# Kernel tuning notes

Hardware: AMD Instinct MI355X
Metric: run time of the kernel (lower is better)

Reference implementation:

```python
import jax, jax.numpy as jnp
import numpy as np

N_USER = 100000
N_SELLER = 50000
E = 640000
D_U = 128
D_S = 64
H = 128
B = 50000


def setup_inputs() -> dict:
    key = jax.random.key(0)
    ks = jax.random.split(key, 24)

    def w(k, shape):
        # Glorot-ish scaling by fan_in
        return jax.random.normal(k, shape, dtype=jnp.float32) / np.sqrt(shape[0])

    return {
        "x_user": jax.random.normal(ks[0], (N_USER, D_U), dtype=jnp.float32),
        "x_seller": jax.random.normal(ks[1], (N_SELLER, D_S), dtype=jnp.float32),
        "src_buy": jax.random.randint(ks[2], (E,), 0, N_USER),
        "dst_buy": jax.random.randint(ks[3], (E,), 0, N_SELLER),
        "src_rev": jax.random.randint(ks[4], (E,), 0, N_SELLER),
        "dst_rev": jax.random.randint(ks[5], (E,), 0, N_USER),
        "mask_user": jax.random.randint(ks[6], (B,), 0, N_USER),
        "mask_seller": jax.random.randint(ks[7], (B,), 0, N_SELLER),
        # layer 1: (user,buy,seller) conv: src=user(D_U), dst=seller(D_S)
        "Wl1_buy": w(ks[8], (D_U, H)), "Wr1_buy": w(ks[9], (D_S, H)),
        "b1_buy": jnp.zeros((H,), jnp.float32),
        # layer 1: (seller,bought by,user) conv: src=seller(D_S), dst=user(D_U)
        "Wl1_rev": w(ks[10], (D_S, H)), "Wr1_rev": w(ks[11], (D_U, H)),
        "b1_rev": jnp.zeros((H,), jnp.float32),
        # layer 2 (both node types now have H features)
        "Wl2_buy": w(ks[12], (H, H)), "Wr2_buy": w(ks[13], (H, H)),
        "b2_buy": jnp.zeros((H,), jnp.float32),
        "Wl2_rev": w(ks[14], (H, H)), "Wr2_rev": w(ks[15], (H, H)),
        "b2_rev": jnp.zeros((H,), jnp.float32),
        # final head: Linear(2H, 1)
        "Wlin": w(ks[16], (2 * H, 1)), "blin": jnp.zeros((1,), jnp.float32),
    }


def _sage(x_src, x_dst, src, dst, Wl, Wr, b):
    """PyG SAGEConv: lin_l(mean_j x_src[j]) + lin_r(x_dst); bias on aggr branch."""
    n_dst = x_dst.shape[0]
    agg = jax.ops.segment_sum(x_src[src], dst, num_segments=n_dst)      # [n_dst, d_src]
    cnt = jax.ops.segment_sum(jnp.ones(src.shape, x_src.dtype), dst, num_segments=n_dst)
    mean = agg / jnp.maximum(cnt, 1.0)[:, None]                          # mean aggr, 0 for isolated
    return mean @ Wl + b + x_dst @ Wr


def reference(x_user, x_seller, src_buy, dst_buy, src_rev, dst_rev,
              mask_user, mask_seller,
              Wl1_buy, Wr1_buy, b1_buy, Wl1_rev, Wr1_rev, b1_rev,
              Wl2_buy, Wr2_buy, b2_buy, Wl2_rev, Wr2_rev, b2_rev,
              Wlin, blin):
    # layer 1 (HeteroConv aggr='sum' is trivial: one relation per dst type)
    s1 = jax.nn.relu(_sage(x_user, x_seller, src_buy, dst_buy, Wl1_buy, Wr1_buy, b1_buy))
    u1 = jax.nn.relu(_sage(x_seller, x_user, src_rev, dst_rev, Wl1_rev, Wr1_rev, b1_rev))
    # layer 2
    s2 = jax.nn.relu(_sage(u1, s1, src_buy, dst_buy, Wl2_buy, Wr2_buy, b2_buy))
    u2 = jax.nn.relu(_sage(s1, u1, src_rev, dst_rev, Wl2_rev, Wr2_rev, b2_rev))
    # masked gather + concat + linear + sigmoid
    x = jnp.concatenate((u2[mask_user], s2[mask_seller]), axis=1)        # [B, 2H]
    return jax.nn.sigmoid(x @ Wlin + blin).reshape(-1)
```

## Files before the change

### kernel.cpp

```cpp
#include <hip/hip_runtime.h>

#define N_USER   100000
#define N_SELLER 50000
#define NEDGE    640000
#define DU       128
#define DS       64
#define HH       128
#define BSZ      50000

#define ECHUNK   2048
#define NBLK     313
#define PW       128
#define NPART_B  391
#define NPART_R  782

#define CVT_BLK  15625
#define PREP_BLK 448

#define NB1_BUY  391
#define NB1_REV  782
#define NB2      391

#define AGG1_BUY_BLK 12500
#define AGG1_REV_BLK 25000
#define AGG2_BLK     12500

typedef unsigned short ushort_t;
typedef __attribute__((ext_vector_type(4))) unsigned short u16x4;
typedef __attribute__((ext_vector_type(8))) unsigned short u16x8;
typedef __attribute__((ext_vector_type(8))) short bf16x8;
typedef __attribute__((ext_vector_type(4))) float f32x4;

__device__ __forceinline__ float bf2f(ushort_t u) {
  union { unsigned int i; float f; } v; v.i = ((unsigned int)u) << 16; return v.f;
}
__device__ __forceinline__ ushort_t f2bf(float f) {
  union { float f; unsigned int i; } v; v.f = f;
  unsigned int x = v.i;
  unsigned int r = x + 0x7FFFu + ((x >> 16) & 1u);
  return (ushort_t)(r >> 16);
}
__device__ __forceinline__ float u2f(unsigned int u) {
  union { unsigned int i; float f; } v; v.i = u; return v.f;
}

__global__ void __launch_bounds__(256) k_hist(
    const int* __restrict__ dst_buy, const int* __restrict__ dst_rev,
    int* __restrict__ H_buy, int* __restrict__ H_rev) {
  __shared__ int lh[NPART_R];
  int b = blockIdx.x, t = threadIdx.x;
  bool is_buy = b < NBLK;
  int bb = is_buy ? b : b - NBLK;
  const int* dst = is_buy ? dst_buy : dst_rev;
  int* H = is_buy ? H_buy : H_rev;
  int np = is_buy ? NPART_B : NPART_R;
  for (int i = t; i < np; i += 256) lh[i] = 0;
  __syncthreads();
  int base = bb * ECHUNK;
#pragma unroll
  for (int i = 0; i < 8; ++i) {
    int e = base + i * 256 + t;
    if (e < NEDGE) atomicAdd(&lh[dst[e] >> 7], 1);
  }
  __syncthreads();
  for (int p = t; p < np; p += 256) H[p * NBLK + bb] = lh[p];
}

__global__ void __launch_bounds__(256) k_rowscan(
    int* __restrict__ H_buy, int* __restrict__ H_rev,
    int* __restrict__ rowtot_buy, int* __restrict__ rowtot_rev) {
  __shared__ int lds[256];
  int p = blockIdx.x, t = threadIdx.x;
  int* H; int* rowtot; int row;
  if (p < NPART_B) { H = H_buy; rowtot = rowtot_buy; row = p; }
  else             { H = H_rev; rowtot = rowtot_rev; row = p - NPART_B; }
  int i0 = 2 * t, i1 = 2 * t + 1;
  int v0 = (i0 < NBLK) ? H[row * NBLK + i0] : 0;
  int v1 = (i1 < NBLK) ? H[row * NBLK + i1] : 0;
  int tot = v0 + v1;
  lds[t] = tot;
  __syncthreads();
  for (int d = 1; d < 256; d <<= 1) {
    int x = (t >= d) ? lds[t - d] : 0;
    __syncthreads();
    lds[t] += x;
    __syncthreads();
  }
  int excl = lds[t] - tot;
  if (i0 < NBLK) H[row * NBLK + i0] = excl;
  if (i1 < NBLK) H[row * NBLK + i1] = excl + v0;
  if (t == 255) rowtot[row] = lds[255];
}

__global__ void __launch_bounds__(256) k_colscan(
    const int* __restrict__ rowtot_buy, const int* __restrict__ rowtot_rev,
    int* __restrict__ pstart_buy, int* __restrict__ pstart_rev) {
  __shared__ int lds[256];
  const int* rt; int* ps; int n;
  if (blockIdx.x == 0) { rt = rowtot_buy; ps = pstart_buy; n = NPART_B; }
  else                 { rt = rowtot_rev; ps = pstart_rev; n = NPART_R; }
  int t = threadIdx.x;
  int v[4]; int tot = 0;
#pragma unroll
  for (int i = 0; i < 4; ++i) { int idx = t * 4 + i; v[i] = (idx < n) ? rt[idx] : 0; tot += v[i]; }
  lds[t] = tot;
  __syncthreads();
  for (int d = 1; d < 256; d <<= 1) {
    int x = (t >= d) ? lds[t - d] : 0;
    __syncthreads();
    lds[t] += x;
    __syncthreads();
  }
  int excl = lds[t] - tot;
#pragma unroll
  for (int i = 0; i < 4; ++i) {
    int idx = t * 4 + i;
    if (idx < n) { ps[idx] = excl; excl += v[i]; }
  }
  if (t == 255) ps[n] = lds[255];
}

__global__ void __launch_bounds__(256) k_scat_cvt_prep(
    const int* __restrict__ src_buy, const int* __restrict__ dst_buy,
    const int* __restrict__ src_rev, const int* __restrict__ dst_rev,
    const int* __restrict__ H_buy, const int* __restrict__ H_rev,
    const int* __restrict__ pstart_buy, const int* __restrict__ pstart_rev,
    unsigned int* __restrict__ part_buy, unsigned int* __restrict__ part_rev,
    const float* __restrict__ x_user, ushort_t* __restrict__ xu_bf,
    const float* __restrict__ x_seller, ushort_t* __restrict__ xs_bf,
    const float* __restrict__ Wl1b, const float* __restrict__ Wr1b, ushort_t* __restrict__ o1b,
    const float* __restrict__ Wl1r, const float* __restrict__ Wr1r, ushort_t* __restrict__ o1r,
    const float* __restrict__ Wl2b, const float* __restrict__ Wr2b, ushort_t* __restrict__ o2b,
    const float* __restrict__ Wl2r, const float* __restrict__ Wr2r, ushort_t* __restrict__ o2r) {
  __shared__ int lc[NPART_R];
  int b = blockIdx.x, t = threadIdx.x;
  if (b < 2 * NBLK) {
    bool is_buy = b < NBLK;
    int bb = is_buy ? b : b - NBLK;
    const int* src = is_buy ? src_buy : src_rev;
    const int* dst = is_buy ? dst_buy : dst_rev;
    const int* H   = is_buy ? H_buy : H_rev;
    const int* ps  = is_buy ? pstart_buy : pstart_rev;
    unsigned int* part = is_buy ? part_buy : part_rev;
    int np = is_buy ? NPART_B : NPART_R;
    for (int i = t; i < np; i += 256) lc[i] = 0;
    __syncthreads();
    int base = bb * ECHUNK;
#pragma unroll
    for (int i = 0; i < 8; ++i) {
      int e = base + i * 256 + t;
      if (e < NEDGE) {
        int d = dst[e], s = src[e];
        int p = d >> 7;
        int r = atomicAdd(&lc[p], 1);
        int pos = ps[p] + H[p * NBLK + bb] + r;
        part[pos] = ((unsigned int)(d & (PW - 1)) << 20) | (unsigned int)s;
      }
    }
  } else if (b < 2 * NBLK + CVT_BLK) {
    int idx = (b - 2 * NBLK) * 256 + t;
    const int na4 = N_USER * DU / 4;
    const float* in; ushort_t* out;
    if (idx < na4) { in = x_user + idx * 4; out = xu_bf + idx * 4; }
    else { idx -= na4; in = x_seller + idx * 4; out = xs_bf + idx * 4; }
    float4 v = *(const float4*)in;
    u16x4 r;
    r.x = f2bf(v.x); r.y = f2bf(v.y); r.z = f2bf(v.z); r.w = f2bf(v.w);
    *(u16x4*)out = r;
  } else {
    int idx = (b - 2 * NBLK - CVT_BLK) * 256 + t;
    const float *Wl, *Wr; ushort_t* out; int D1;
    if (idx < 24576)      { Wl = Wl1b; Wr = Wr1b; out = o1b; D1 = 128; }
    else if (idx < 49152) { idx -= 24576; Wl = Wl1r; Wr = Wr1r; out = o1r; D1 = 64; }
    else if (idx < 81920) { idx -= 49152; Wl = Wl2b; Wr = Wr2b; out = o2b; D1 = 128; }
    else                  { idx -= 81920; Wl = Wl2r; Wr = Wr2r; out = o2r; D1 = 128; }
    int f = idx >> 9;
    int r = idx & 511;
    int l = r >> 3;
    int j = r & 7;
    int kcidx = f >> 3;
    int c = f & 7;
    int h = (l & 15) + c * 16;
    int k = kcidx * 32 + (l >> 4) * 8 + j;
    float w = (k < D1) ? Wl[k * HH + h] : Wr[(k - D1) * HH + h];
    out[idx] = f2bf(w);
  }
}

__global__ void __launch_bounds__(256) k_csr(
    const unsigned int* __restrict__ part_buy, const unsigned int* __restrict__ part_rev,
    const int* __restrict__ pstart_buy, const int* __restrict__ pstart_rev,
    int* __restrict__ off_buy, int* __restrict__ off_rev,
    int* __restrict__ csr_buy, int* __restrict__ csr_rev) {
  __shared__ int lcnt[PW], loff[PW], sc[PW];
  int B = blockIdx.x, t = threadIdx.x;
  bool is_buy = B < NPART_B;
  int p = is_buy ? B : B - NPART_B;
  const unsigned int* part = is_buy ? part_buy : part_rev;
  const int* ps = is_buy ? pstart_buy : pstart_rev;
  int* off = is_buy ? off_buy : off_rev;
  int* csr = is_buy ? csr_buy : csr_rev;
  int nnode = is_buy ? N_SELLER : N_USER;
  int s0 = ps[p], s1 = ps[p + 1];
  if (t < PW) lcnt[t] = 0;
  __syncthreads();
  for (int e = s0 + t; e < s1; e += 256) {
    int d = (int)(part[e] >> 20);
    atomicAdd(&lcnt[d], 1);
  }
  __syncthreads();
  int v = (t < PW) ? lcnt[t] : 0;
  if (t < PW) sc[t] = v;
  __syncthreads();
  for (int d = 1; d < PW; d <<= 1) {
    int x = (t >= d && t < PW) ? sc[t - d] : 0;
    __syncthreads();
    if (t < PW) sc[t] += x;
    __syncthreads();
  }
  if (t < PW) {
    loff[t] = sc[t] - v;
    int node = p * PW + t;
    if (node < nnode) off[node] = s0 + loff[t];
    lcnt[t] = 0;
  }
  if (B == 0 && t == 0) { off_buy[N_SELLER] = NEDGE; off_rev[N_USER] = NEDGE; }
  __syncthreads();
  for (int e = s0 + t; e < s1; e += 256) {
    unsigned int pk = part[e];
    int l = (int)(pk >> 20);
    int r = atomicAdd(&lcnt[l], 1);
    csr[s0 + loff[l] + r] = (int)(pk & 0xFFFFFu);
  }
}

template <int D, int U>
__device__ __forceinline__ void agg_body(
    int blk, const ushort_t* __restrict__ X,
    const int* __restrict__ off, const int* __restrict__ csr,
    const int* __restrict__ idxs, int nrows,
    ushort_t* __restrict__ out) {
  constexpr int LPR = D / 8;
  constexpr int EPW = 64 / LPR;
  int wave = threadIdx.x >> 6;
  int lane = threadIdx.x & 63;
  int n = blk * 4 + wave;
  if (n >= nrows) return;
  int node = idxs ? idxs[n] : n;
  int g = lane / LPR;
  int c = (lane % LPR) * 8;
  int i0 = off[node], i1 = off[node + 1];
  const ushort_t* Xc = X + c;

  float2 acc[4];
#pragma unroll
  for (int q = 0; q < 4; ++q) acc[q] = (float2){0.f, 0.f};

  int i = i0 + g;
  for (; i + (U - 1) * EPW < i1; i += U * EPW) {
    int idxv[U];
#pragma unroll
    for (int u = 0; u < U; ++u) idxv[u] = csr[i + u * EPW];
    uint4 v[U];
#pragma unroll
    for (int u = 0; u < U; ++u)
      v[u] = *(const uint4*)(Xc + (size_t)idxv[u] * D);
#pragma unroll
    for (int u = 0; u < U; ++u) {
      acc[0] += (float2){u2f(v[u].x << 16), u2f(v[u].x & 0xFFFF0000u)};
      acc[1] += (float2){u2f(v[u].y << 16), u2f(v[u].y & 0xFFFF0000u)};
      acc[2] += (float2){u2f(v[u].z << 16), u2f(v[u].z & 0xFFFF0000u)};
      acc[3] += (float2){u2f(v[u].w << 16), u2f(v[u].w & 0xFFFF0000u)};
    }
  }
  for (; i < i1; i += EPW) {
    int s = csr[i];
    uint4 v = *(const uint4*)(Xc + (size_t)s * D);
    acc[0] += (float2){u2f(v.x << 16), u2f(v.x & 0xFFFF0000u)};
    acc[1] += (float2){u2f(v.y << 16), u2f(v.y & 0xFFFF0000u)};
    acc[2] += (float2){u2f(v.z << 16), u2f(v.z & 0xFFFF0000u)};
    acc[3] += (float2){u2f(v.w << 16), u2f(v.w & 0xFFFF0000u)};
  }

#pragma unroll
  for (int mm = LPR; mm < 64; mm <<= 1) {
#pragma unroll
    for (int q = 0; q < 4; ++q) {
      acc[q].x += __shfl_xor(acc[q].x, mm);
      acc[q].y += __shfl_xor(acc[q].y, mm);
    }
  }

  if (g == 0) {
    int deg = i1 - i0;
    float inv = 1.f / (float)(deg > 0 ? deg : 1);
    u16x8 r;
#pragma unroll
    for (int q = 0; q < 4; ++q) {
      r[2 * q]     = f2bf(acc[q].x * inv);
      r[2 * q + 1] = f2bf(acc[q].y * inv);
    }
    *(u16x8*)(out + (size_t)n * D + c) = r;
  }
}

__global__ void __launch_bounds__(256) agg_layer1(
    const ushort_t* __restrict__ xu_bf, const ushort_t* __restrict__ xs_bf,
    const int* __restrict__ off_buy, const int* __restrict__ csr_buy,
    const int* __restrict__ off_rev, const int* __restrict__ csr_rev,
    ushort_t* __restrict__ mean_buy, ushort_t* __restrict__ mean_rev) {
  int b = blockIdx.x;
  if (b < AGG1_BUY_BLK)
    agg_body<128, 2>(b, xu_bf, off_buy, csr_buy, nullptr, N_SELLER, mean_buy);
  else
    agg_body<64, 2>(b - AGG1_BUY_BLK, xs_bf, off_rev, csr_rev, nullptr, N_USER, mean_rev);
}

__global__ void __launch_bounds__(256) agg_layer2(
    const ushort_t* __restrict__ u1, const ushort_t* __restrict__ s1,
    const int* __restrict__ off_buy, const int* __restrict__ csr_buy,
    const int* __restrict__ off_rev, const int* __restrict__ csr_rev,
    const int* __restrict__ mask_seller, const int* __restrict__ mask_user,
    ushort_t* __restrict__ mean_buy, ushort_t* __restrict__ mean_rev) {
  int b = blockIdx.x;
  if (b < AGG2_BLK)
    agg_body<128, 2>(b, u1, off_buy, csr_buy, mask_seller, BSZ, mean_buy);
  else
    agg_body<128, 2>(b - AGG2_BLK, s1, off_rev, csr_rev, mask_user, BSZ, mean_rev);
}

template <int K, bool HEAD>
__device__ __forceinline__ void gemm_body(
    int blk, ushort_t* lds,
    const ushort_t* __restrict__ A1, int ld1, int D1, const int* __restrict__ mask1,
    const ushort_t* __restrict__ A2, int ld2, const int* __restrict__ mask2,
    const ushort_t* __restrict__ Wf, const float* __restrict__ bias,
    ushort_t* __restrict__ out, float* __restrict__ partial,
    const float* __restrict__ wlin_seg, int M) {
  constexpr int NCH = K / 32;
  int t = threadIdx.x;
  int wave = t >> 6;
  int lane = t & 63;

  constexpr int ITERS = (HH * K * 2) / 4096;
#pragma unroll
  for (int i = 0; i < ITERS; ++i) {
    const ushort_t* g = Wf + i * 2048 + t * 8;
    ushort_t* l = lds + i * 2048 + wave * 512;
    __builtin_amdgcn_global_load_lds((const __attribute__((address_space(1))) void*)g,
                                     (__attribute__((address_space(3))) void*)l, 16, 0, 0);
  }

  int row0 = blk * 128 + wave * 32;
  int kb = (lane >> 4) << 3;
  bf16x8 af[2][NCH];
#pragma unroll
  for (int s = 0; s < 2; ++s) {
    int r = row0 + s * 16 + (lane & 15);
    int rsafe = r < M ? r : M - 1;
    int a1 = mask1 ? mask1[rsafe] : rsafe;
    int a2 = mask2 ? mask2[rsafe] : rsafe;
#pragma unroll
    for (int kc = 0; kc < NCH; ++kc) {
      int k = kc * 32 + kb;
      const ushort_t* ap = (k < D1) ? (A1 + (size_t)a1 * ld1 + k)
                                    : (A2 + (size_t)a2 * ld2 + (k - D1));
      af[s][kc] = *(const bf16x8*)ap;
    }
  }

  f32x4 acc[2][8];
#pragma unroll
  for (int s = 0; s < 2; ++s)
#pragma unroll
    for (int c = 0; c < 8; ++c) acc[s][c] = (f32x4){0.f, 0.f, 0.f, 0.f};

  __syncthreads();

#pragma unroll
  for (int kc = 0; kc < NCH; ++kc) {
#pragma unroll
    for (int c = 0; c < 8; ++c) {
      bf16x8 bf = *(const bf16x8*)(lds + ((kc * 8 + c) * 512 + lane * 8));
      acc[0][c] = __builtin_amdgcn_mfma_f32_16x16x32_bf16(af[0][kc], bf, acc[0][c], 0, 0, 0);
      acc[1][c] = __builtin_amdgcn_mfma_f32_16x16x32_bf16(af[1][kc], bf, acc[1][c], 0, 0, 0);
    }
  }

  int colb = lane & 15;
  if constexpr (!HEAD) {
#pragma unroll
    for (int s = 0; s < 2; ++s) {
      int rbase = row0 + s * 16 + ((lane >> 4) << 2);
#pragma unroll
      for (int c = 0; c < 8; ++c) {
        int col = c * 16 + colb;
        float bv = bias[col];
#pragma unroll
        for (int j = 0; j < 4; ++j) {
          int rout = rbase + j;
          if (rout < M) {
            float v = fmaxf(acc[s][c][j] + bv, 0.f);
            out[(size_t)rout * HH + col] = f2bf(v);
          }
        }
      }
    }
  } else {
    float wl[8], bv[8];
#pragma unroll
    for (int c = 0; c < 8; ++c) {
      wl[c] = wlin_seg[c * 16 + colb];
      bv[c] = bias[c * 16 + colb];
    }
#pragma unroll
    for (int s = 0; s < 2; ++s) {
      float p0 = 0.f, p1 = 0.f, p2 = 0.f, p3 = 0.f;
#pragma unroll
      for (int c = 0; c < 8; ++c) {
        p0 += fmaxf(acc[s][c][0] + bv[c], 0.f) * wl[c];
        p1 += fmaxf(acc[s][c][1] + bv[c], 0.f) * wl[c];
        p2 += fmaxf(acc[s][c][2] + bv[c], 0.f) * wl[c];
        p3 += fmaxf(acc[s][c][3] + bv[c], 0.f) * wl[c];
      }
#pragma unroll
      for (int m = 1; m < 16; m <<= 1) {
        p0 += __shfl_xor(p0, m);
        p1 += __shfl_xor(p1, m);
        p2 += __shfl_xor(p2, m);
        p3 += __shfl_xor(p3, m);
      }
      if (colb == 0) {
        int rbase = row0 + s * 16 + ((lane >> 4) << 2);
        if (rbase + 0 < M) partial[rbase + 0] = p0;
        if (rbase + 1 < M) partial[rbase + 1] = p1;
        if (rbase + 2 < M) partial[rbase + 2] = p2;
        if (rbase + 3 < M) partial[rbase + 3] = p3;
      }
    }
  }
}

__global__ void __launch_bounds__(256) gemm_layer1(
    const ushort_t* __restrict__ mean_buy, const ushort_t* __restrict__ xs_bf,
    const ushort_t* __restrict__ mean_rev, const ushort_t* __restrict__ xu_bf,
    const ushort_t* __restrict__ wt1_buy, const float* __restrict__ b1_buy,
    const ushort_t* __restrict__ wt1_rev, const float* __restrict__ b1_rev,
    ushort_t* __restrict__ s1, ushort_t* __restrict__ u1) {
  __shared__ ushort_t lds[HH * 192];
  int b = blockIdx.x;
  if (b < NB1_BUY)
    gemm_body<192, false>(b, lds, mean_buy, 128, 128, nullptr, xs_bf, 64, nullptr,
                          wt1_buy, b1_buy, s1, nullptr, nullptr, N_SELLER);
  else
    gemm_body<192, false>(b - NB1_BUY, lds, mean_rev, 64, 64, nullptr, xu_bf, 128, nullptr,
                          wt1_rev, b1_rev, u1, nullptr, nullptr, N_USER);
}

__global__ void __launch_bounds__(256) gemm_layer2(
    const ushort_t* __restrict__ mean_buy, const ushort_t* __restrict__ s1,
    const ushort_t* __restrict__ mean_rev, const ushort_t* __restrict__ u1,
    const int* __restrict__ mask_seller, const int* __restrict__ mask_user,
    const ushort_t* __restrict__ wt2_buy, const float* __restrict__ b2_buy,
    const ushort_t* __restrict__ wt2_rev, const float* __restrict__ b2_rev,
    const float* __restrict__ wlin,
    float* __restrict__ ps, float* __restrict__ pu) {
  __shared__ ushort_t lds[HH * 256];
  int b = blockIdx.x;
  if (b < NB2)
    gemm_body<256, true>(b, lds, mean_buy, 128, 128, nullptr, s1, 128, mask_seller,
                         wt2_buy, b2_buy, nullptr, ps, wlin + 128, BSZ);
  else
    gemm_body<256, true>(b - NB2, lds, mean_rev, 128, 128, nullptr, u1, 128, mask_user,
                         wt2_rev, b2_rev, nullptr, pu, wlin, BSZ);
}

__global__ void head_fin(const float* __restrict__ pu, const float* __restrict__ ps,
                         const float* __restrict__ blin, float* __restrict__ out) {
  int i = blockIdx.x * 256 + threadIdx.x;
  if (i < BSZ) {
    float z = pu[i] + ps[i] + blin[0];
    out[i] = 1.f / (1.f + expf(-z));
  }
}

extern "C" void kernel_launch(void* const* d_in, const int* in_sizes, int n_in,
                              void* d_out, int out_size, void* d_ws, size_t ws_size,
                              hipStream_t stream) {
  const float* x_user    = (const float*)d_in[0];
  const float* x_seller  = (const float*)d_in[1];
  const int* src_buy  = (const int*)d_in[2];
  const int* dst_buy  = (const int*)d_in[3];
  const int* src_rev  = (const int*)d_in[4];
  const int* dst_rev  = (const int*)d_in[5];
  const int* mask_user   = (const int*)d_in[6];
  const int* mask_seller = (const int*)d_in[7];
  const float* Wl1_buy = (const float*)d_in[8];
  const float* Wr1_buy = (const float*)d_in[9];
  const float* b1_buy  = (const float*)d_in[10];
  const float* Wl1_rev = (const float*)d_in[11];
  const float* Wr1_rev = (const float*)d_in[12];
  const float* b1_rev  = (const float*)d_in[13];
  const float* Wl2_buy = (const float*)d_in[14];
  const float* Wr2_buy = (const float*)d_in[15];
  const float* b2_buy  = (const float*)d_in[16];
  const float* Wl2_rev = (const float*)d_in[17];
  const float* Wr2_rev = (const float*)d_in[18];
  const float* b2_rev  = (const float*)d_in[19];
  const float* Wlin    = (const float*)d_in[20];
  const float* blin    = (const float*)d_in[21];

  char* ws = (char*)d_ws;
  size_t o = 0;
  auto alloc = [&](size_t bytes) { size_t p = o; o += (bytes + 255) & ~(size_t)255; return p; };
  size_t wt1_buy_o = alloc(HH * 192 * 2);
  size_t wt1_rev_o = alloc(HH * 192 * 2);
  size_t wt2_buy_o = alloc(HH * 256 * 2);
  size_t wt2_rev_o = alloc(HH * 256 * 2);
  size_t H_buy_o = alloc((size_t)NPART_B * NBLK * 4);
  size_t H_rev_o = alloc((size_t)NPART_R * NBLK * 4);
  size_t rowtot_buy_o = alloc(NPART_B * 4);
  size_t rowtot_rev_o = alloc(NPART_R * 4);
  size_t pstart_buy_o = alloc((NPART_B + 1) * 4);
  size_t pstart_rev_o = alloc((NPART_R + 1) * 4);
  size_t part_buy_o = alloc((size_t)NEDGE * 4);
  size_t part_rev_o = alloc((size_t)NEDGE * 4);
  size_t off_buy_o = alloc((size_t)(N_SELLER + 1) * 4);
  size_t off_rev_o = alloc((size_t)(N_USER + 1) * 4);
  size_t csr_buy_o = alloc((size_t)NEDGE * 4);
  size_t csr_rev_o = alloc((size_t)NEDGE * 4);
  size_t xu_bf_o = alloc((size_t)N_USER * DU * 2);
  size_t xs_bf_o = alloc((size_t)N_SELLER * DS * 2);
  size_t mean_buy_o = alloc((size_t)N_SELLER * 128 * 2);
  size_t mean_rev_o = alloc((size_t)N_USER * 64 * 2);
  size_t s1_o = alloc((size_t)N_SELLER * HH * 2);
  size_t u1_o = alloc((size_t)N_USER * HH * 2);
  size_t ps_o = alloc((size_t)50048 * 4);
  size_t pu_o = alloc((size_t)50048 * 4);
  (void)ws_size;

  ushort_t* wt1_buy = (ushort_t*)(ws + wt1_buy_o);
  ushort_t* wt1_rev = (ushort_t*)(ws + wt1_rev_o);
  ushort_t* wt2_buy = (ushort_t*)(ws + wt2_buy_o);
  ushort_t* wt2_rev = (ushort_t*)(ws + wt2_rev_o);
  int* H_buy = (int*)(ws + H_buy_o);
  int* H_rev = (int*)(ws + H_rev_o);
  int* rowtot_buy = (int*)(ws + rowtot_buy_o);
  int* rowtot_rev = (int*)(ws + rowtot_rev_o);
  int* pstart_buy = (int*)(ws + pstart_buy_o);
  int* pstart_rev = (int*)(ws + pstart_rev_o);
  unsigned int* part_buy = (unsigned int*)(ws + part_buy_o);
  unsigned int* part_rev = (unsigned int*)(ws + part_rev_o);
  int* off_buy = (int*)(ws + off_buy_o);
  int* off_rev = (int*)(ws + off_rev_o);
  int* csr_buy = (int*)(ws + csr_buy_o);
  int* csr_rev = (int*)(ws + csr_rev_o);
  ushort_t* xu_bf = (ushort_t*)(ws + xu_bf_o);
  ushort_t* xs_bf = (ushort_t*)(ws + xs_bf_o);
  ushort_t* mean_buy = (ushort_t*)(ws + mean_buy_o);
  ushort_t* mean_rev = (ushort_t*)(ws + mean_rev_o);
  ushort_t* s1 = (ushort_t*)(ws + s1_o);
  ushort_t* u1 = (ushort_t*)(ws + u1_o);
  float* ps = (float*)(ws + ps_o);
  float* pu = (float*)(ws + pu_o);

  k_hist<<<2 * NBLK, 256, 0, stream>>>(dst_buy, dst_rev, H_buy, H_rev);
  k_rowscan<<<NPART_B + NPART_R, 256, 0, stream>>>(H_buy, H_rev, rowtot_buy, rowtot_rev);
  k_colscan<<<2, 256, 0, stream>>>(rowtot_buy, rowtot_rev, pstart_buy, pstart_rev);
  k_scat_cvt_prep<<<2 * NBLK + CVT_BLK + PREP_BLK, 256, 0, stream>>>(
      src_buy, dst_buy, src_rev, dst_rev, H_buy, H_rev, pstart_buy, pstart_rev,
      part_buy, part_rev,
      x_user, xu_bf, x_seller, xs_bf,
      Wl1_buy, Wr1_buy, wt1_buy, Wl1_rev, Wr1_rev, wt1_rev,
      Wl2_buy, Wr2_buy, wt2_buy, Wl2_rev, Wr2_rev, wt2_rev);
  k_csr<<<NPART_B + NPART_R, 256, 0, stream>>>(part_buy, part_rev, pstart_buy, pstart_rev,
                                               off_buy, off_rev, csr_buy, csr_rev);

  agg_layer1<<<AGG1_BUY_BLK + AGG1_REV_BLK, 256, 0, stream>>>(
      xu_bf, xs_bf, off_buy, csr_buy, off_rev, csr_rev, mean_buy, mean_rev);
  gemm_layer1<<<NB1_BUY + NB1_REV, 256, 0, stream>>>(
      mean_buy, xs_bf, mean_rev, xu_bf, wt1_buy, b1_buy, wt1_rev, b1_rev, s1, u1);

  agg_layer2<<<AGG2_BLK + AGG2_BLK, 256, 0, stream>>>(
      u1, s1, off_buy, csr_buy, off_rev, csr_rev, mask_seller, mask_user,
      mean_buy, mean_rev);
  gemm_layer2<<<NB2 + NB2, 256, 0, stream>>>(
      mean_buy, s1, mean_rev, u1, mask_seller, mask_user,
      wt2_buy, b2_buy, wt2_rev, b2_rev, Wlin, ps, pu);

  head_fin<<<(BSZ + 255) / 256, 256, 0, stream>>>(pu, ps, blin, (float*)d_out);
}
```

Measured before the change: 203.3 us.

## Deduplicate masked nodes before layer-2 aggregation and GEMM

Builds unique lists of masked seller and user nodes with atomic dedup, plus inverse maps. Layer-2 aggregation and GEMM then run only over the unique nodes, and the head gathers results through the inverse index. This cuts redundant layer-2 work for repeated mask entries. It also moves the CSR build into the conversion/prep kernel, so the launch sequence changes. The cost is extra memsets, atomics and an indirection pass.

```diff
diff --git a/kernel.cpp b/kernel.cpp
--- a/kernel.cpp
+++ b/kernel.cpp
@@ -13,9 +13,11 @@
 #define PW       128
 #define NPART_B  391
 #define NPART_R  782
+#define NCSR     (NPART_B + NPART_R)
 
 #define CVT_BLK  15625
 #define PREP_BLK 448
+#define DED_BLK  391
 
 #define NB1_BUY  391
 #define NB1_REV  782
@@ -44,52 +46,85 @@
   union { unsigned int i; float f; } v; v.i = u; return v.f;
 }
 
-__global__ void __launch_bounds__(256) k_hist(
+__global__ void __launch_bounds__(256) k_hist_dedup(
     const int* __restrict__ dst_buy, const int* __restrict__ dst_rev,
-    int* __restrict__ H_buy, int* __restrict__ H_rev) {
+    int* __restrict__ H_buy, int* __restrict__ H_rev,
+    const int* __restrict__ mask_seller, const int* __restrict__ mask_user,
+    int* __restrict__ seen_s, int* __restrict__ seen_u,
+    int* __restrict__ map_s, int* __restrict__ map_u,
+    int* __restrict__ uniq_s, int* __restrict__ uniq_u,
+    int* __restrict__ nu) {
   __shared__ int lh[NPART_R];
   int b = blockIdx.x, t = threadIdx.x;
-  bool is_buy = b < NBLK;
-  int bb = is_buy ? b : b - NBLK;
-  const int* dst = is_buy ? dst_buy : dst_rev;
-  int* H = is_buy ? H_buy : H_rev;
-  int np = is_buy ? NPART_B : NPART_R;
-  for (int i = t; i < np; i += 256) lh[i] = 0;
-  __syncthreads();
-  int base = bb * ECHUNK;
-#pragma unroll
-  for (int i = 0; i < 8; ++i) {
-    int e = base + i * 256 + t;
-    if (e < NEDGE) atomicAdd(&lh[dst[e] >> 7], 1);
-  }
-  __syncthreads();
-  for (int p = t; p < np; p += 256) H[p * NBLK + bb] = lh[p];
-}
-
-__global__ void __launch_bounds__(256) k_rowscan(
+  if (b < 2 * NBLK) {
+    bool is_buy = b < NBLK;
+    int bb = is_buy ? b : b - NBLK;
+    const int* dst = is_buy ? dst_buy : dst_rev;
+    int* H = is_buy ? H_buy : H_rev;
+    int np = is_buy ? NPART_B : NPART_R;
+    for (int i = t; i < np; i += 256) lh[i] = 0;
+    __syncthreads();
+    int base = bb * ECHUNK;
+#pragma unroll
+    for (int i = 0; i < 8; ++i) {
+      int e = base + i * 256 + t;
+      if (e < NEDGE) atomicAdd(&lh[dst[e] >> 7], 1);
+    }
+    __syncthreads();
+    for (int p = t; p < np; p += 256) H[p * NBLK + bb] = lh[p];
+  } else {
+    int i = (b - 2 * NBLK) * 256 + t;
+    if (i < BSZ) {
+      int node = mask_seller[i];
+      if (atomicExch(&seen_s[node], 1) == 0) {
+        int uid = atomicAdd(&nu[0], 1);
+        map_s[node] = uid;
+        uniq_s[uid] = node;
+      }
+    } else if (i < 2 * BSZ) {
+      int node = mask_user[i - BSZ];
+      if (atomicExch(&seen_u[node], 1) == 0) {
+        int uid = atomicAdd(&nu[1], 1);
+        map_u[node] = uid;
+        uniq_u[uid] = node;
+      }
+    }
+  }
+}
+
+__global__ void __launch_bounds__(256) k_rowscan_inv(
     int* __restrict__ H_buy, int* __restrict__ H_rev,
-    int* __restrict__ rowtot_buy, int* __restrict__ rowtot_rev) {
+    int* __restrict__ rowtot_buy, int* __restrict__ rowtot_rev,
+    const int* __restrict__ mask_seller, const int* __restrict__ mask_user,
+    const int* __restrict__ map_s, const int* __restrict__ map_u,
+    int* __restrict__ inv_s, int* __restrict__ inv_u) {
   __shared__ int lds[256];
   int p = blockIdx.x, t = threadIdx.x;
-  int* H; int* rowtot; int row;
-  if (p < NPART_B) { H = H_buy; rowtot = rowtot_buy; row = p; }
-  else             { H = H_rev; rowtot = rowtot_rev; row = p - NPART_B; }
-  int i0 = 2 * t, i1 = 2 * t + 1;
-  int v0 = (i0 < NBLK) ? H[row * NBLK + i0] : 0;
-  int v1 = (i1 < NBLK) ? H[row * NBLK + i1] : 0;
-  int tot = v0 + v1;
-  lds[t] = tot;
-  __syncthreads();
-  for (int d = 1; d < 256; d <<= 1) {
-    int x = (t >= d) ? lds[t - d] : 0;
-    __syncthreads();
-    lds[t] += x;
-    __syncthreads();
-  }
-  int excl = lds[t] - tot;
-  if (i0 < NBLK) H[row * NBLK + i0] = excl;
-  if (i1 < NBLK) H[row * NBLK + i1] = excl + v0;
-  if (t == 255) rowtot[row] = lds[255];
+  if (p < NCSR) {
+    int* H; int* rowtot; int row;
+    if (p < NPART_B) { H = H_buy; rowtot = rowtot_buy; row = p; }
+    else             { H = H_rev; rowtot = rowtot_rev; row = p - NPART_B; }
+    int i0 = 2 * t, i1 = 2 * t + 1;
+    int v0 = (i0 < NBLK) ? H[row * NBLK + i0] : 0;
+    int v1 = (i1 < NBLK) ? H[row * NBLK + i1] : 0;
+    int tot = v0 + v1;
+    lds[t] = tot;
+    __syncthreads();
+    for (int d = 1; d < 256; d <<= 1) {
+      int x = (t >= d) ? lds[t - d] : 0;
+      __syncthreads();
+      lds[t] += x;
+      __syncthreads();
+    }
+    int excl = lds[t] - tot;
+    if (i0 < NBLK) H[row * NBLK + i0] = excl;
+    if (i1 < NBLK) H[row * NBLK + i1] = excl + v0;
+    if (t == 255) rowtot[row] = lds[255];
+  } else {
+    int i = (p - NCSR) * 256 + t;
+    if (i < BSZ) inv_s[i] = map_s[mask_seller[i]];
+    else if (i < 2 * BSZ) inv_u[i - BSZ] = map_u[mask_user[i - BSZ]];
+  }
 }
 
 __global__ void __launch_bounds__(256) k_colscan(
@@ -120,45 +155,92 @@
   if (t == 255) ps[n] = lds[255];
 }
 
-__global__ void __launch_bounds__(256) k_scat_cvt_prep(
+__global__ void __launch_bounds__(256) k_scat(
     const int* __restrict__ src_buy, const int* __restrict__ dst_buy,
     const int* __restrict__ src_rev, const int* __restrict__ dst_rev,
     const int* __restrict__ H_buy, const int* __restrict__ H_rev,
     const int* __restrict__ pstart_buy, const int* __restrict__ pstart_rev,
-    unsigned int* __restrict__ part_buy, unsigned int* __restrict__ part_rev,
+    unsigned int* __restrict__ part_buy, unsigned int* __restrict__ part_rev) {
+  __shared__ int lc[NPART_R];
+  int b = blockIdx.x, t = threadIdx.x;
+  bool is_buy = b < NBLK;
+  int bb = is_buy ? b : b - NBLK;
+  const int* src = is_buy ? src_buy : src_rev;
+  const int* dst = is_buy ? dst_buy : dst_rev;
+  const int* H   = is_buy ? H_buy : H_rev;
+  const int* ps  = is_buy ? pstart_buy : pstart_rev;
+  unsigned int* part = is_buy ? part_buy : part_rev;
+  int np = is_buy ? NPART_B : NPART_R;
+  for (int i = t; i < np; i += 256) lc[i] = 0;
+  __syncthreads();
+  int base = bb * ECHUNK;
+#pragma unroll
+  for (int i = 0; i < 8; ++i) {
+    int e = base + i * 256 + t;
+    if (e < NEDGE) {
+      int d = dst[e], s = src[e];
+      int p = d >> 7;
+      int r = atomicAdd(&lc[p], 1);
+      int pos = ps[p] + H[p * NBLK + bb] + r;
+      part[pos] = ((unsigned int)(d & (PW - 1)) << 20) | (unsigned int)s;
+    }
+  }
+}
+
+__global__ void __launch_bounds__(256) k_csr_cvt_prep(
+    const unsigned int* __restrict__ part_buy, const unsigned int* __restrict__ part_rev,
+    const int* __restrict__ pstart_buy, const int* __restrict__ pstart_rev,
+    int* __restrict__ off_buy, int* __restrict__ off_rev,
+    int* __restrict__ csr_buy, int* __restrict__ csr_rev,
     const float* __restrict__ x_user, ushort_t* __restrict__ xu_bf,
     const float* __restrict__ x_seller, ushort_t* __restrict__ xs_bf,
     const float* __restrict__ Wl1b, const float* __restrict__ Wr1b, ushort_t* __restrict__ o1b,
     const float* __restrict__ Wl1r, const float* __restrict__ Wr1r, ushort_t* __restrict__ o1r,
     const float* __restrict__ Wl2b, const float* __restrict__ Wr2b, ushort_t* __restrict__ o2b,
     const float* __restrict__ Wl2r, const float* __restrict__ Wr2r, ushort_t* __restrict__ o2r) {
-  __shared__ int lc[NPART_R];
-  int b = blockIdx.x, t = threadIdx.x;
-  if (b < 2 * NBLK) {
-    bool is_buy = b < NBLK;
-    int bb = is_buy ? b : b - NBLK;
-    const int* src = is_buy ? src_buy : src_rev;
-    const int* dst = is_buy ? dst_buy : dst_rev;
-    const int* H   = is_buy ? H_buy : H_rev;
-    const int* ps  = is_buy ? pstart_buy : pstart_rev;
-    unsigned int* part = is_buy ? part_buy : part_rev;
-    int np = is_buy ? NPART_B : NPART_R;
-    for (int i = t; i < np; i += 256) lc[i] = 0;
-    __syncthreads();
-    int base = bb * ECHUNK;
-#pragma unroll
-    for (int i = 0; i < 8; ++i) {
-      int e = base + i * 256 + t;
-      if (e < NEDGE) {
-        int d = dst[e], s = src[e];
-        int p = d >> 7;
-        int r = atomicAdd(&lc[p], 1);
-        int pos = ps[p] + H[p * NBLK + bb] + r;
-        part[pos] = ((unsigned int)(d & (PW - 1)) << 20) | (unsigned int)s;
-      }
-    }
-  } else if (b < 2 * NBLK + CVT_BLK) {
-    int idx = (b - 2 * NBLK) * 256 + t;
+  __shared__ int lcnt[PW], loff[PW], sc[PW];
+  int B = blockIdx.x, t = threadIdx.x;
+  if (B < NCSR) {
+    bool is_buy = B < NPART_B;
+    int p = is_buy ? B : B - NPART_B;
+    const unsigned int* part = is_buy ? part_buy : part_rev;
+    const int* ps = is_buy ? pstart_buy : pstart_rev;
+    int* off = is_buy ? off_buy : off_rev;
+    int* csr = is_buy ? csr_buy : csr_rev;
+    int nnode = is_buy ? N_SELLER : N_USER;
+    int s0 = ps[p], s1 = ps[p + 1];
+    if (t < PW) lcnt[t] = 0;
+    __syncthreads();
+    for (int e = s0 + t; e < s1; e += 256) {
+      int d = (int)(part[e] >> 20);
+      atomicAdd(&lcnt[d], 1);
+    }
+    __syncthreads();
+    int v = (t < PW) ? lcnt[t] : 0;
+    if (t < PW) sc[t] = v;
+    __syncthreads();
+    for (int d = 1; d < PW; d <<= 1) {
+      int x = (t >= d && t < PW) ? sc[t - d] : 0;
+      __syncthreads();
+      if (t < PW) sc[t] += x;
+      __syncthreads();
+    }
+    if (t < PW) {
+      loff[t] = sc[t] - v;
+      int node = p * PW + t;
+      if (node < nnode) off[node] = s0 + loff[t];
+      lcnt[t] = 0;
+    }
+    if (B == 0 && t == 0) { off_buy[N_SELLER] = NEDGE; off_rev[N_USER] = NEDGE; }
+    __syncthreads();
+    for (int e = s0 + t; e < s1; e += 256) {
+      unsigned int pk = part[e];
+      int l = (int)(pk >> 20);
+      int r = atomicAdd(&lcnt[l], 1);
+      csr[s0 + loff[l] + r] = (int)(pk & 0xFFFFFu);
+    }
+  } else if (B < NCSR + CVT_BLK) {
+    int idx = (B - NCSR) * 256 + t;
     const int na4 = N_USER * DU / 4;
     const float* in; ushort_t* out;
     if (idx < na4) { in = x_user + idx * 4; out = xu_bf + idx * 4; }
@@ -168,7 +250,7 @@
     r.x = f2bf(v.x); r.y = f2bf(v.y); r.z = f2bf(v.z); r.w = f2bf(v.w);
     *(u16x4*)out = r;
   } else {
-    int idx = (b - 2 * NBLK - CVT_BLK) * 256 + t;
+    int idx = (B - NCSR - CVT_BLK) * 256 + t;
     const float *Wl, *Wr; ushort_t* out; int D1;
     if (idx < 24576)      { Wl = Wl1b; Wr = Wr1b; out = o1b; D1 = 128; }
     else if (idx < 49152) { idx -= 24576; Wl = Wl1r; Wr = Wr1r; out = o1r; D1 = 64; }
@@ -184,53 +266,6 @@
     int k = kcidx * 32 + (l >> 4) * 8 + j;
     float w = (k < D1) ? Wl[k * HH + h] : Wr[(k - D1) * HH + h];
     out[idx] = f2bf(w);
-  }
-}
-
-__global__ void __launch_bounds__(256) k_csr(
-    const unsigned int* __restrict__ part_buy, const unsigned int* __restrict__ part_rev,
-    const int* __restrict__ pstart_buy, const int* __restrict__ pstart_rev,
-    int* __restrict__ off_buy, int* __restrict__ off_rev,
-    int* __restrict__ csr_buy, int* __restrict__ csr_rev) {
-  __shared__ int lcnt[PW], loff[PW], sc[PW];
-  int B = blockIdx.x, t = threadIdx.x;
-  bool is_buy = B < NPART_B;
-  int p = is_buy ? B : B - NPART_B;
-  const unsigned int* part = is_buy ? part_buy : part_rev;
-  const int* ps = is_buy ? pstart_buy : pstart_rev;
-  int* off = is_buy ? off_buy : off_rev;
-  int* csr = is_buy ? csr_buy : csr_rev;
-  int nnode = is_buy ? N_SELLER : N_USER;
-  int s0 = ps[p], s1 = ps[p + 1];
-  if (t < PW) lcnt[t] = 0;
-  __syncthreads();
-  for (int e = s0 + t; e < s1; e += 256) {
-    int d = (int)(part[e] >> 20);
-    atomicAdd(&lcnt[d], 1);
-  }
-  __syncthreads();
-  int v = (t < PW) ? lcnt[t] : 0;
-  if (t < PW) sc[t] = v;
-  __syncthreads();
-  for (int d = 1; d < PW; d <<= 1) {
-    int x = (t >= d && t < PW) ? sc[t - d] : 0;
-    __syncthreads();
-    if (t < PW) sc[t] += x;
-    __syncthreads();
-  }
-  if (t < PW) {
-    loff[t] = sc[t] - v;
-    int node = p * PW + t;
-    if (node < nnode) off[node] = s0 + loff[t];
-    lcnt[t] = 0;
-  }
-  if (B == 0 && t == 0) { off_buy[N_SELLER] = NEDGE; off_rev[N_USER] = NEDGE; }
-  __syncthreads();
-  for (int e = s0 + t; e < s1; e += 256) {
-    unsigned int pk = part[e];
-    int l = (int)(pk >> 20);
-    int r = atomicAdd(&lcnt[l], 1);
-    csr[s0 + loff[l] + r] = (int)(pk & 0xFFFFFu);
   }
 }
 
@@ -320,13 +355,14 @@
     const ushort_t* __restrict__ u1, const ushort_t* __restrict__ s1,
     const int* __restrict__ off_buy, const int* __restrict__ csr_buy,
     const int* __restrict__ off_rev, const int* __restrict__ csr_rev,
-    const int* __restrict__ mask_seller, const int* __restrict__ mask_user,
+    const int* __restrict__ uniq_s, const int* __restrict__ uniq_u,
+    const int* __restrict__ nu,
     ushort_t* __restrict__ mean_buy, ushort_t* __restrict__ mean_rev) {
   int b = blockIdx.x;
   if (b < AGG2_BLK)
-    agg_body<128, 2>(b, u1, off_buy, csr_buy, mask_seller, BSZ, mean_buy);
+    agg_body<128, 2>(b, u1, off_buy, csr_buy, uniq_s, nu[0], mean_buy);
   else
-    agg_body<128, 2>(b - AGG2_BLK, s1, off_rev, csr_rev, mask_user, BSZ, mean_rev);
+    agg_body<128, 2>(b - AGG2_BLK, s1, off_rev, csr_rev, uniq_u, nu[1], mean_rev);
 }
 
 template <int K, bool HEAD>
@@ -460,26 +496,34 @@
 __global__ void __launch_bounds__(256) gemm_layer2(
     const ushort_t* __restrict__ mean_buy, const ushort_t* __restrict__ s1,
     const ushort_t* __restrict__ mean_rev, const ushort_t* __restrict__ u1,
-    const int* __restrict__ mask_seller, const int* __restrict__ mask_user,
+    const int* __restrict__ uniq_s, const int* __restrict__ uniq_u,
+    const int* __restrict__ nu,
     const ushort_t* __restrict__ wt2_buy, const float* __restrict__ b2_buy,
     const ushort_t* __restrict__ wt2_rev, const float* __restrict__ b2_rev,
     const float* __restrict__ wlin,
     float* __restrict__ ps, float* __restrict__ pu) {
   __shared__ ushort_t lds[HH * 256];
   int b = blockIdx.x;
-  if (b < NB2)
-    gemm_body<256, true>(b, lds, mean_buy, 128, 128, nullptr, s1, 128, mask_seller,
-                         wt2_buy, b2_buy, nullptr, ps, wlin + 128, BSZ);
-  else
-    gemm_body<256, true>(b - NB2, lds, mean_rev, 128, 128, nullptr, u1, 128, mask_user,
-                         wt2_rev, b2_rev, nullptr, pu, wlin, BSZ);
+  if (b < NB2) {
+    int M = nu[0];
+    if (b * 128 >= M) return;
+    gemm_body<256, true>(b, lds, mean_buy, 128, 128, nullptr, s1, 128, uniq_s,
+                         wt2_buy, b2_buy, nullptr, ps, wlin + 128, M);
+  } else {
+    int M = nu[1];
+    int bb = b - NB2;
+    if (bb * 128 >= M) return;
+    gemm_body<256, true>(bb, lds, mean_rev, 128, 128, nullptr, u1, 128, uniq_u,
+                         wt2_rev, b2_rev, nullptr, pu, wlin, M);
+  }
 }
 
 __global__ void head_fin(const float* __restrict__ pu, const float* __restrict__ ps,
+                         const int* __restrict__ inv_u, const int* __restrict__ inv_s,
                          const float* __restrict__ blin, float* __restrict__ out) {
   int i = blockIdx.x * 256 + threadIdx.x;
   if (i < BSZ) {
-    float z = pu[i] + ps[i] + blin[0];
+    float z = pu[inv_u[i]] + ps[inv_s[i]] + blin[0];
     out[i] = 1.f / (1.f + expf(-z));
   }
 }
@@ -537,6 +581,15 @@
   size_t u1_o = alloc((size_t)N_USER * HH * 2);
   size_t ps_o = alloc((size_t)50048 * 4);
   size_t pu_o = alloc((size_t)50048 * 4);
+  size_t seen_s_o = alloc((size_t)N_SELLER * 4);
+  size_t seen_u_o = alloc((size_t)N_USER * 4);
+  size_t map_s_o  = alloc((size_t)N_SELLER * 4);
+  size_t map_u_o  = alloc((size_t)N_USER * 4);
+  size_t uniq_s_o = alloc((size_t)BSZ * 4);
+  size_t uniq_u_o = alloc((size_t)BSZ * 4);
+  size_t inv_s_o  = alloc((size_t)BSZ * 4);
+  size_t inv_u_o  = alloc((size_t)BSZ * 4);
+  size_t nu_o     = alloc(2 * 4);
   (void)ws_size;
 
   ushort_t* wt1_buy = (ushort_t*)(ws + wt1_buy_o);
@@ -563,18 +616,35 @@
   ushort_t* u1 = (ushort_t*)(ws + u1_o);
   float* ps = (float*)(ws + ps_o);
   float* pu = (float*)(ws + pu_o);
-
-  k_hist<<<2 * NBLK, 256, 0, stream>>>(dst_buy, dst_rev, H_buy, H_rev);
-  k_rowscan<<<NPART_B + NPART_R, 256, 0, stream>>>(H_buy, H_rev, rowtot_buy, rowtot_rev);
+  int* seen_s = (int*)(ws + seen_s_o);
+  int* seen_u = (int*)(ws + seen_u_o);
+  int* map_s  = (int*)(ws + map_s_o);
+  int* map_u  = (int*)(ws + map_u_o);
+  int* uniq_s = (int*)(ws + uniq_s_o);
+  int* uniq_u = (int*)(ws + uniq_u_o);
+  int* inv_s  = (int*)(ws + inv_s_o);
+  int* inv_u  = (int*)(ws + inv_u_o);
+  int* nu     = (int*)(ws + nu_o);
+
+  hipMemsetAsync(seen_s, 0, (size_t)N_SELLER * 4, stream);
+  hipMemsetAsync(seen_u, 0, (size_t)N_USER * 4, stream);
+  hipMemsetAsync(nu, 0, 8, stream);
+  k_hist_dedup<<<2 * NBLK + DED_BLK, 256, 0, stream>>>(
+      dst_buy, dst_rev, H_buy, H_rev,
+      mask_seller, mask_user, seen_s, seen_u, map_s, map_u, uniq_s, uniq_u, nu);
+  k_rowscan_inv<<<NCSR + DED_BLK, 256, 0, stream>>>(
+      H_buy, H_rev, rowtot_buy, rowtot_rev,
+      mask_seller, mask_user, map_s, map_u, inv_s, inv_u);
   k_colscan<<<2, 256, 0, stream>>>(rowtot_buy, rowtot_rev, pstart_buy, pstart_rev);
-  k_scat_cvt_prep<<<2 * NBLK + CVT_BLK + PREP_BLK, 256, 0, stream>>>(
-      src_buy, dst_buy, src_rev, dst_rev, H_buy, H_rev, pstart_buy, pstart_rev,
-      part_buy, part_rev,
+  k_scat<<<2 * NBLK, 256, 0, stream>>>(src_buy, dst_buy, src_rev, dst_rev,
+                                       H_buy, H_rev, pstart_buy, pstart_rev,
+                                       part_buy, part_rev);
+  k_csr_cvt_prep<<<NCSR + CVT_BLK + PREP_BLK, 256, 0, stream>>>(
+      part_buy, part_rev, pstart_buy, pstart_rev,
+      off_buy, off_rev, csr_buy, csr_rev,
       x_user, xu_bf, x_seller, xs_bf,
       Wl1_buy, Wr1_buy, wt1_buy, Wl1_rev, Wr1_rev, wt1_rev,
       Wl2_buy, Wr2_buy, wt2_buy, Wl2_rev, Wr2_rev, wt2_rev);
-  k_csr<<<NPART_B + NPART_R, 256, 0, stream>>>(part_buy, part_rev, pstart_buy, pstart_rev,
-                                               off_buy, off_rev, csr_buy, csr_rev);
 
   agg_layer1<<<AGG1_BUY_BLK + AGG1_REV_BLK, 256, 0, stream>>>(
       xu_bf, xs_bf, off_buy, csr_buy, off_rev, csr_rev, mean_buy, mean_rev);
@@ -582,11 +652,11 @@
       mean_buy, xs_bf, mean_rev, xu_bf, wt1_buy, b1_buy, wt1_rev, b1_rev, s1, u1);
 
   agg_layer2<<<AGG2_BLK + AGG2_BLK, 256, 0, stream>>>(
-      u1, s1, off_buy, csr_buy, off_rev, csr_rev, mask_seller, mask_user,
+      u1, s1, off_buy, csr_buy, off_rev, csr_rev, uniq_s, uniq_u, nu,
       mean_buy, mean_rev);
   gemm_layer2<<<NB2 + NB2, 256, 0, stream>>>(
-      mean_buy, s1, mean_rev, u1, mask_seller, mask_user,
+      mean_buy, s1, mean_rev, u1, uniq_s, uniq_u, nu,
       wt2_buy, b2_buy, wt2_rev, b2_rev, Wlin, ps, pu);
 
-  head_fin<<<(BSZ + 255) / 256, 256, 0, stream>>>(pu, ps, blin, (float*)d_out);
-}
+  head_fin<<<(BSZ + 255) / 256, 256, 0, stream>>>(pu, ps, inv_u, inv_s, blin, (float*)d_out);
+}
```

New measurement: 213.9 us. +5.2%, slower.
